# Kernel tuning notes

Hardware: AMD Instinct MI355X
Metric: run time of the kernel (lower is better)

The kernel has to match this reference:

```python
import jax, jax.numpy as jnp
import numpy as np

N = 50000      # nodes
E = 1000000    # edges (avg degree 20)
IN, H, OUT = 3, 128, 3


def setup_inputs() -> dict:
    key = jax.random.key(0)
    ks = jax.random.split(key, 12)
    pos = jax.random.normal(ks[0], (N, IN), dtype=jnp.float32)
    edge_index = jax.random.randint(ks[1], (2, E), 0, N, dtype=jnp.int64)
    dims = [(IN, H), (H, H), (H, H), (H, H), (H, OUT)]
    inp = {"pos": pos, "edge_index": edge_index}
    for i, (di, do) in enumerate(dims):
        inp[f"W{i}"] = jax.random.normal(ks[2 + 2 * i], (di, do), dtype=jnp.float32) / np.sqrt(di).astype(np.float32)
        inp[f"b{i}"] = jnp.zeros((do,), dtype=jnp.float32)
    return inp


def _gcn_conv(x, W, b, src, dst, norm):
    # PyG GCNConv: linear transform first, then normalized scatter-add, then bias
    h = x @ W                                  # [N, do]
    msg = h[src] * norm[:, None]               # gather + edge-normalize  [E+N, do]
    out = jax.ops.segment_sum(msg, dst, num_segments=N)  # scatter-add to targets
    return out + b


def reference(pos, edge_index, W0, b0, W1, b1, W2, b2, W3, b3, W4, b4):
    src, dst = edge_index[0], edge_index[1]
    loop = jnp.arange(N, dtype=src.dtype)
    src = jnp.concatenate([src, loop])         # add self-loops
    dst = jnp.concatenate([dst, loop])
    # symmetric normalization: deg computed on target nodes incl. self-loops
    deg = jax.ops.segment_sum(jnp.ones_like(src, dtype=pos.dtype), dst, num_segments=N)
    dis = jnp.where(deg > 0, jax.lax.rsqrt(jnp.maximum(deg, 1e-12)), 0.0)
    norm = dis[src] * dis[dst]                 # [E+N]

    Ws = [W0, W1, W2, W3, W4]
    bs = [b0, b1, b2, b3, b4]
    x = pos
    for i in range(4):                         # all but last layer: conv + SiLU
        x = jax.nn.silu(_gcn_conv(x, Ws[i], bs[i], src, dst, norm))
    return _gcn_conv(x, Ws[4], bs[4], src, dst, norm)
```

## Files before the change

### kernel.cpp

```cpp
#include <hip/hip_runtime.h>
#include <cstdint>
#include <cstddef>


#define NB_SPLIT 256
#define BUCKET_SHIFT 7

static __device__ __forceinline__ float silu_f(float x) {
  return x / (1.0f + __expf(-x));
}

__global__ __launch_bounds__(256) void k_prep(
    const int* __restrict__ e32, int* __restrict__ epack, int* __restrict__ cnt2,
    int E, int nbucket, int chunk) {
  __shared__ int hist[512];
  __shared__ int nz;
  const int w = blockIdx.x, t = threadIdx.x;
  for (int b = t; b < nbucket; b += 256) hist[b] = 0;
  if (t == 0) nz = 0;
  __syncthreads();
  if (e32[t * 2 + 1] != 0) nz = 1;
  __syncthreads();
  const int f = nz ? 0 : 1;
  const int i0 = w * chunk;
  const int i1 = min(E, i0 + chunk);
  for (int i = i0 + t; i < i1; i += 256) {
    int s, d;
    if (f) { s = e32[2 * i]; d = e32[2 * E + 2 * i]; }
    else   { s = e32[i];     d = e32[E + i]; }
    epack[i] = s | (d << 16);
    atomicAdd(&hist[d >> BUCKET_SHIFT], 1);
  }
  __syncthreads();
  for (int b = t; b < nbucket; b += 256) cnt2[b * NB_SPLIT + w] = hist[b];
}

__global__ void k_scan1(const int* __restrict__ cnt, int* __restrict__ outp,
                        int* __restrict__ bsum, int n) {
  __shared__ int wsum[4];
  const int t = threadIdx.x;
  const int base = blockIdx.x * 1024 + t * 4;
  int v0 = 0, v1 = 0, v2 = 0, v3 = 0;
  if (base + 0 < n) v0 = cnt[base + 0];
  if (base + 1 < n) v1 = cnt[base + 1];
  if (base + 2 < n) v2 = cnt[base + 2];
  if (base + 3 < n) v3 = cnt[base + 3];
  const int s = v0 + v1 + v2 + v3;
  int sc = s;
  const int lane = t & 63;
  #pragma unroll
  for (int o = 1; o < 64; o <<= 1) {
    int u = __shfl_up(sc, o);
    if (lane >= o) sc += u;
  }
  const int wid = t >> 6;
  if (lane == 63) wsum[wid] = sc;
  __syncthreads();
  int wbase = 0;
  for (int w = 0; w < wid; ++w) wbase += wsum[w];
  const int ex = wbase + sc - s;
  if (base + 0 < n) outp[base + 0] = ex;
  if (base + 1 < n) outp[base + 1] = ex + v0;
  if (base + 2 < n) outp[base + 2] = ex + v0 + v1;
  if (base + 3 < n) outp[base + 3] = ex + v0 + v1 + v2;
  if (t == 0) bsum[blockIdx.x] = wsum[0] + wsum[1] + wsum[2] + wsum[3];
}

__global__ __launch_bounds__(512) void k_sscan(
    int* __restrict__ arr, int n, int* __restrict__ tot0, int* __restrict__ tot1) {
  __shared__ int wsum[8];
  const int t = threadIdx.x;
  int v = (t < n) ? arr[t] : 0;
  int sc = v;
  const int lane = t & 63;
  #pragma unroll
  for (int o = 1; o < 64; o <<= 1) {
    int u = __shfl_up(sc, o);
    if (lane >= o) sc += u;
  }
  if (lane == 63) wsum[t >> 6] = sc;
  __syncthreads();
  int wb = 0;
  const int wid = t >> 6;
  for (int w = 0; w < wid; ++w) wb += wsum[w];
  const int ex = wb + sc - v;
  if (t < n) arr[t] = ex;
  if (t == n - 1) {
    int total = ex + v;
    if (tot0) *tot0 = total;
    if (tot1) *tot1 = total;
  }
}

__global__ void k_scanadd(int* __restrict__ arr, const int* __restrict__ bsum, int n) {
  int i = blockIdx.x * blockDim.x + threadIdx.x;
  if (i < n) arr[i] += bsum[i >> 10];
}

__global__ __launch_bounds__(256) void k_split(
    const int* __restrict__ epack, const int* __restrict__ off2,
    int* __restrict__ tmp, int E, int nbucket, int chunk) {
  __shared__ int cur[512];
  const int w = blockIdx.x, t = threadIdx.x;
  for (int b = t; b < nbucket; b += 256) cur[b] = off2[b * NB_SPLIT + w];
  __syncthreads();
  const int i0 = w * chunk;
  const int i1 = min(E, i0 + chunk);
  for (int i = i0 + t; i < i1; i += 256) {
    int p = epack[i];
    int b = (int)(((unsigned)p) >> (16 + BUCKET_SHIFT));
    int pos = atomicAdd(&cur[b], 1);
    tmp[pos] = p;
  }
}

__global__ __launch_bounds__(256) void k_csrA(
    const int* __restrict__ tmp, const int* __restrict__ off2,
    int* __restrict__ cnt_g, int* __restrict__ bpad, int E, int nbucket) {
  __shared__ int lcnt[128];
  __shared__ int tot;
  const int b = blockIdx.x, t = threadIdx.x;
  if (t < 128) lcnt[t] = 0;
  if (t == 0) tot = 0;
  __syncthreads();
  const int s0 = off2[b * NB_SPLIT];
  const int s1 = (b + 1 < nbucket) ? off2[(b + 1) * NB_SPLIT] : E;
  for (int i = s0 + t; i < s1; i += 256) {
    atomicAdd(&lcnt[((unsigned)tmp[i] >> 16) & 127u], 1);
  }
  __syncthreads();
  if (t < 128) {
    int v = lcnt[t];
    cnt_g[b * 128 + t] = v;
    atomicAdd(&tot, (v + 3) & ~3);
  }
  __syncthreads();
  if (t == 0) bpad[b] = tot;
}

__global__ __launch_bounds__(256) void k_csrB(
    const int* __restrict__ tmp, const int* __restrict__ off2,
    const int* __restrict__ cnt_g, const int* __restrict__ bpad,
    int* __restrict__ rowp, float* __restrict__ dis,
    unsigned short* __restrict__ col, int E, int nbucket, int N) {
  __shared__ int lcur[128];
  __shared__ int wtot;
  const int b = blockIdx.x, t = threadIdx.x;
  const int nb0 = b << BUCKET_SHIFT;
  const int nn = min(1 << BUCKET_SHIFT, N - nb0);
  int v = 0, pv = 0, sc = 0;
  if (t < 128) {
    v = cnt_g[b * 128 + t];
    pv = (v + 3) & ~3;
    sc = pv;
    #pragma unroll
    for (int o = 1; o < 64; o <<= 1) {
      int u = __shfl_up(sc, o);
      if ((t & 63) >= o) sc += u;
    }
    if (t == 63) wtot = sc;
  }
  __syncthreads();
  if (t < 128) {
    int ex = bpad[b] + ((t >= 64) ? wtot : 0) + sc - pv;
    lcur[t] = ex;
    if (t < nn) {
      rowp[nb0 + t] = ex;
      dis[nb0 + t] = rsqrtf((float)(v + 1));
      for (int p = ex + v; p < ex + pv; ++p) col[p] = (unsigned short)N;
    }
  }
  __syncthreads();
  const int s0 = off2[b * NB_SPLIT];
  const int s1 = (b + 1 < nbucket) ? off2[(b + 1) * NB_SPLIT] : E;
  for (int i = s0 + t; i < s1; i += 256) {
    unsigned p = (unsigned)tmp[i];
    int j = (int)((p >> 16) & ((1u << BUCKET_SHIFT) - 1));
    int pos = atomicAdd(&lcur[j], 1);
    col[pos] = (unsigned short)(p & 0xffffu);
  }
}

__global__ void k_zfill(float* __restrict__ bufA, float* __restrict__ bufB,
                        int N, int slStride) {
  const int t = threadIdx.x;
  const int bi = t >> 7, si = (t >> 4) & 7, ci = t & 15;
  float* bp = bi ? bufB : bufA;
  bp[(size_t)si * slStride + (size_t)N * 16 + ci] = 0.f;
}

template <int PRESCALE>
__global__ void k_agg3(const float* __restrict__ in3, float* __restrict__ out3,
                       const int* __restrict__ rowp,
                       const unsigned short* __restrict__ col,
                       const float* __restrict__ dis, const float* __restrict__ bias,
                       int n) {
  int i = blockIdx.x * blockDim.x + threadIdx.x;
  if (i >= n) return;
  const float di = dis[i];
  float a0, a1, a2;
  if (PRESCALE) {
    a0 = in3[i * 3 + 0] * di; a1 = in3[i * 3 + 1] * di; a2 = in3[i * 3 + 2] * di;
  } else {
    a0 = in3[i * 3 + 0]; a1 = in3[i * 3 + 1]; a2 = in3[i * 3 + 2];
  }
  const int e0 = rowp[i], e1 = rowp[i + 1];
  for (int e = e0; e < e1; ++e) {
    int s = col[e];
    if (s >= n) continue;
    if (PRESCALE) {
      float ds_ = dis[s];
      a0 += in3[s * 3 + 0] * ds_;
      a1 += in3[s * 3 + 1] * ds_;
      a2 += in3[s * 3 + 2] * ds_;
    } else {
      a0 += in3[s * 3 + 0];
      a1 += in3[s * 3 + 1];
      a2 += in3[s * 3 + 2];
    }
  }
  a0 *= di; a1 *= di; a2 *= di;
  if (!PRESCALE && bias) { a0 += bias[0]; a1 += bias[1]; a2 += bias[2]; }
  out3[i * 3 + 0] = a0;
  out3[i * 3 + 1] = a1;
  out3[i * 3 + 2] = a2;
}

__global__ void k_mm0(const float* __restrict__ y3, const float* __restrict__ W0,
                      const float* __restrict__ b0, const float* __restrict__ dis,
                      float* __restrict__ out, int n, int slStride) {
  int gid = blockIdx.x * blockDim.x + threadIdx.x;
  int node = gid >> 5;
  int c = (gid & 31) << 2;
  if (node >= n) return;
  float v0 = y3[node * 3 + 0], v1 = y3[node * 3 + 1], v2 = y3[node * 3 + 2];
  float4 a  = *reinterpret_cast<const float4*>(b0 + c);
  float4 w0 = *reinterpret_cast<const float4*>(W0 + 0 * 128 + c);
  float4 w1 = *reinterpret_cast<const float4*>(W0 + 1 * 128 + c);
  float4 w2 = *reinterpret_cast<const float4*>(W0 + 2 * 128 + c);
  a.x += v0 * w0.x + v1 * w1.x + v2 * w2.x;
  a.y += v0 * w0.y + v1 * w1.y + v2 * w2.y;
  a.z += v0 * w0.z + v1 * w1.z + v2 * w2.z;
  a.w += v0 * w0.w + v1 * w1.w + v2 * w2.w;
  const float d = dis[node];
  a.x = silu_f(a.x) * d; a.y = silu_f(a.y) * d;
  a.z = silu_f(a.z) * d; a.w = silu_f(a.w) * d;
  *reinterpret_cast<float4*>(out + (size_t)(c >> 4) * slStride +
                             (size_t)node * 16 + (c & 15)) = a;
}

__global__ __launch_bounds__(256) void k_agg_slice(
    const float* __restrict__ xs, float* __restrict__ y,
    const int* __restrict__ rowp, const unsigned short* __restrict__ col,
    const float* __restrict__ dis, int n, int slStride) {
  const int s = blockIdx.x & 7;
  const int nb = blockIdx.x >> 3;
  const int t = threadIdx.x;
  const int lane = t & 63;
  const int nsub = lane >> 3;
  const int ch = (lane >> 2) & 1;
  const int c4 = (lane & 3) << 2;
  const int node = nb * 32 + (t >> 6) * 8 + nsub;
  const bool valid = node < n;
  int e0 = 0, e1 = 0;
  if (valid) { e0 = rowp[node]; e1 = rowp[node + 1]; }
  const int P = e1 - e0;
  const int h = ((P >> 1) + 3) & ~3;
  const int eb = e0 + (ch ? h : 0);
  const int ee = ch ? e1 : (e0 + h);
  const float* __restrict__ xb = xs + (size_t)s * slStride + c4;

  float4 a0 = make_float4(0.f, 0.f, 0.f, 0.f);
  float4 a1 = make_float4(0.f, 0.f, 0.f, 0.f);
  float4 a2 = make_float4(0.f, 0.f, 0.f, 0.f);
  float4 a3 = make_float4(0.f, 0.f, 0.f, 0.f);
  for (int e = eb; e < ee; e += 4) {
    ushort4 idx = *reinterpret_cast<const ushort4*>(col + e);
    float4 v0 = *reinterpret_cast<const float4*>(xb + (size_t)idx.x * 16);
    float4 v1 = *reinterpret_cast<const float4*>(xb + (size_t)idx.y * 16);
    float4 v2 = *reinterpret_cast<const float4*>(xb + (size_t)idx.z * 16);
    float4 v3 = *reinterpret_cast<const float4*>(xb + (size_t)idx.w * 16);
    a0.x += v0.x; a0.y += v0.y; a0.z += v0.z; a0.w += v0.w;
    a1.x += v1.x; a1.y += v1.y; a1.z += v1.z; a1.w += v1.w;
    a2.x += v2.x; a2.y += v2.y; a2.z += v2.z; a2.w += v2.w;
    a3.x += v3.x; a3.y += v3.y; a3.z += v3.z; a3.w += v3.w;
  }
  a0.x += a1.x + a2.x + a3.x;
  a0.y += a1.y + a2.y + a3.y;
  a0.z += a1.z + a2.z + a3.z;
  a0.w += a1.w + a2.w + a3.w;
  a0.x += __shfl_xor(a0.x, 4);
  a0.y += __shfl_xor(a0.y, 4);
  a0.z += __shfl_xor(a0.z, 4);
  a0.w += __shfl_xor(a0.w, 4);
  if (valid && ch == 0) {
    float4 self = *reinterpret_cast<const float4*>(xb + (size_t)node * 16);
    const float d = dis[node];
    float4 r;
    r.x = (a0.x + self.x) * d;
    r.y = (a0.y + self.y) * d;
    r.z = (a0.z + self.z) * d;
    r.w = (a0.w + self.w) * d;
    *reinterpret_cast<float4*>(y + (size_t)s * slStride + (size_t)node * 16 + c4) = r;
  }
}

template <int PROJ>
__global__ __launch_bounds__(512, 4) void k_mm_w(
    const float* __restrict__ x, const float* __restrict__ W,
    const float* __restrict__ bias, const float* __restrict__ dis,
    float* __restrict__ out, const float* __restrict__ W4, int n, int slStride) {
  __shared__ float ws[128][128];
  const int t = threadIdx.x;
  #pragma unroll
  for (int it = 0; it < 8; ++it) {
    int i = t + it * 512;
    int k = i >> 5, b = i & 31;
    int slot = (b >> 1) | ((b & 1) << 4);
    *reinterpret_cast<float4*>(&ws[k][slot << 2]) =
        *reinterpret_cast<const float4*>(W + (size_t)i * 4);
  }
  __syncthreads();

  const int tc = t & 15;
  const int tr = (t >> 4) << 2;
  const int row0 = blockIdx.x * 128;

  int rb[4];
  #pragma unroll
  for (int r = 0; r < 4; ++r) {
    rb[r] = min(row0 + tr + r, n - 1) * 16;
  }

  float4 accA[4], accB[4];
  #pragma unroll
  for (int r = 0; r < 4; ++r) {
    accA[r] = make_float4(0.f, 0.f, 0.f, 0.f);
    accB[r] = make_float4(0.f, 0.f, 0.f, 0.f);
  }

  #pragma unroll 1
  for (int kk = 0; kk < 128; kk += 4) {
    const float* __restrict__ xk = x + (size_t)(kk >> 4) * slStride + (kk & 15);
    float4 xr[4];
    #pragma unroll
    for (int r = 0; r < 4; ++r) {
      xr[r] = *reinterpret_cast<const float4*>(xk + rb[r]);
    }
    #pragma unroll
    for (int j = 0; j < 4; ++j) {
      float4 wA = *reinterpret_cast<const float4*>(&ws[kk + j][tc << 2]);
      float4 wB = *reinterpret_cast<const float4*>(&ws[kk + j][64 + (tc << 2)]);
      #pragma unroll
      for (int r = 0; r < 4; ++r) {
        float xv = (j == 0) ? xr[r].x : (j == 1) ? xr[r].y : (j == 2) ? xr[r].z : xr[r].w;
        accA[r].x += xv * wA.x; accA[r].y += xv * wA.y;
        accA[r].z += xv * wA.z; accA[r].w += xv * wA.w;
        accB[r].x += xv * wB.x; accB[r].y += xv * wB.y;
        accB[r].z += xv * wB.z; accB[r].w += xv * wB.w;
      }
    }
  }

  float4 bbA = *reinterpret_cast<const float4*>(bias + tc * 8);
  float4 bbB = *reinterpret_cast<const float4*>(bias + tc * 8 + 4);
  if (PROJ) {
    float w4r[8][3];
    #pragma unroll
    for (int c = 0; c < 8; ++c) {
      w4r[c][0] = W4[(tc * 8 + c) * 3 + 0];
      w4r[c][1] = W4[(tc * 8 + c) * 3 + 1];
      w4r[c][2] = W4[(tc * 8 + c) * 3 + 2];
    }
    #pragma unroll
    for (int r = 0; r < 4; ++r) {
      int row = row0 + tr + r;
      float d = (row < n) ? dis[row] : 0.0f;
      float4 a = accA[r], b4 = accB[r];
      a.x = silu_f(a.x + bbA.x) * d;  a.y = silu_f(a.y + bbA.y) * d;
      a.z = silu_f(a.z + bbA.z) * d;  a.w = silu_f(a.w + bbA.w) * d;
      b4.x = silu_f(b4.x + bbB.x) * d; b4.y = silu_f(b4.y + bbB.y) * d;
      b4.z = silu_f(b4.z + bbB.z) * d; b4.w = silu_f(b4.w + bbB.w) * d;
      float p0 = a.x * w4r[0][0] + a.y * w4r[1][0] + a.z * w4r[2][0] + a.w * w4r[3][0]
               + b4.x * w4r[4][0] + b4.y * w4r[5][0] + b4.z * w4r[6][0] + b4.w * w4r[7][0];
      float p1 = a.x * w4r[0][1] + a.y * w4r[1][1] + a.z * w4r[2][1] + a.w * w4r[3][1]
               + b4.x * w4r[4][1] + b4.y * w4r[5][1] + b4.z * w4r[6][1] + b4.w * w4r[7][1];
      float p2 = a.x * w4r[0][2] + a.y * w4r[1][2] + a.z * w4r[2][2] + a.w * w4r[3][2]
               + b4.x * w4r[4][2] + b4.y * w4r[5][2] + b4.z * w4r[6][2] + b4.w * w4r[7][2];
      #pragma unroll
      for (int m = 8; m >= 1; m >>= 1) {
        p0 += __shfl_xor(p0, m);
        p1 += __shfl_xor(p1, m);
        p2 += __shfl_xor(p2, m);
      }
      if ((t & 15) == 0 && row < n) {
        out[row * 3 + 0] = p0;
        out[row * 3 + 1] = p1;
        out[row * 3 + 2] = p2;
      }
    }
  } else {
    #pragma unroll
    for (int r = 0; r < 4; ++r) {
      int row = row0 + tr + r;
      if (row < n) {
        float d = dis[row];
        float4 a = accA[r], b4 = accB[r];
        a.x = silu_f(a.x + bbA.x) * d;  a.y = silu_f(a.y + bbA.y) * d;
        a.z = silu_f(a.z + bbA.z) * d;  a.w = silu_f(a.w + bbA.w) * d;
        b4.x = silu_f(b4.x + bbB.x) * d; b4.y = silu_f(b4.y + bbB.y) * d;
        b4.z = silu_f(b4.z + bbB.z) * d; b4.w = silu_f(b4.w + bbB.w) * d;
        float* dst = out + (size_t)(tc >> 1) * slStride +
                     (size_t)row * 16 + ((tc & 1) << 3);
        *reinterpret_cast<float4*>(dst) = a;
        *reinterpret_cast<float4*>(dst + 4) = b4;
      }
    }
  }
}

extern "C" void kernel_launch(void* const* d_in, const int* in_sizes, int n_in,
                              void* d_out, int out_size, void* d_ws, size_t ws_size,
                              hipStream_t stream) {
  const float* pos = (const float*)d_in[0];
  const int* e32 = (const int*)d_in[1];
  const float* W[5] = {(const float*)d_in[2], (const float*)d_in[4], (const float*)d_in[6],
                       (const float*)d_in[8], (const float*)d_in[10]};
  const float* B[5] = {(const float*)d_in[3], (const float*)d_in[5], (const float*)d_in[7],
                       (const float*)d_in[9], (const float*)d_in[11]};
  float* out = (float*)d_out;

  const int N = in_sizes[0] / 3;
  const int E = in_sizes[1] / 2;
  const int NBUCKET = (N + (1 << BUCKET_SHIFT) - 1) >> BUCKET_SHIFT;
  const int M = NBUCKET * NB_SPLIT;
  const int chunk = (E + NB_SPLIT - 1) / NB_SPLIT;
  const int slStride = (N + 1) * 16;

  char* base = (char*)d_ws;
  size_t off = 0;
  auto alloc = [&](size_t bytes) -> void* {
    void* p = base + off;
    off += (bytes + 255) & ~(size_t)255;
    return p;
  };
  float* dis   = (float*)alloc((size_t)N * 4);
  int* rowp    = (int*)alloc((size_t)(N + 1) * 4);
  int* bsum2   = (int*)alloc(128 * 4);
  int* cnt_g   = (int*)alloc((size_t)NBUCKET * 128 * 4);
  int* bpad    = (int*)alloc((size_t)(NBUCKET + 1) * 4);
  int* cnt2    = (int*)alloc((size_t)M * 4);
  int* off2    = (int*)alloc((size_t)M * 4);
  unsigned short* col = (unsigned short*)alloc(((size_t)E + 4 * N) * 2);
  float* y3    = (float*)alloc((size_t)N * 3 * 4);
  float* bufA  = (float*)alloc((size_t)(N + 1) * 128 * 4);
  float* bufB  = (float*)alloc((size_t)(N + 1) * 128 * 4);
  int* epack = (int*)bufA;
  int* tmp   = (int*)bufB;

  const int nblk2 = (M + 1023) / 1024;

  k_prep<<<NB_SPLIT, 256, 0, stream>>>(e32, epack, cnt2, E, NBUCKET, chunk);
  k_scan1<<<nblk2, 256, 0, stream>>>(cnt2, off2, bsum2, M);
  k_sscan<<<1, 512, 0, stream>>>(bsum2, nblk2, nullptr, nullptr);
  k_scanadd<<<(M + 255) / 256, 256, 0, stream>>>(off2, bsum2, M);
  k_split<<<NB_SPLIT, 256, 0, stream>>>(epack, off2, tmp, E, NBUCKET, chunk);
  k_csrA<<<NBUCKET, 256, 0, stream>>>(tmp, off2, cnt_g, bpad, E, NBUCKET);
  k_sscan<<<1, 512, 0, stream>>>(bpad, NBUCKET, bpad + NBUCKET, rowp + N);
  k_csrB<<<NBUCKET, 256, 0, stream>>>(tmp, off2, cnt_g, bpad, rowp, dis, col, E, NBUCKET, N);
  k_zfill<<<1, 256, 0, stream>>>(bufA, bufB, N, slStride);

  k_agg3<1><<<(N + 255) / 256, 256, 0, stream>>>(pos, y3, rowp, col, dis, nullptr, N);
  k_mm0<<<(N * 32 + 255) / 256, 256, 0, stream>>>(y3, W[0], B[0], dis, bufA, N, slStride);

  const int agg_grid = ((N + 31) / 32) * 8;
  const int mm_grid = (N + 127) / 128;
  for (int l = 1; l <= 2; ++l) {
    k_agg_slice<<<agg_grid, 256, 0, stream>>>(bufA, bufB, rowp, col, dis, N, slStride);
    k_mm_w<0><<<mm_grid, 512, 0, stream>>>(bufB, W[l], B[l], dis, bufA, nullptr, N, slStride);
  }

  k_agg_slice<<<agg_grid, 256, 0, stream>>>(bufA, bufB, rowp, col, dis, N, slStride);
  k_mm_w<1><<<mm_grid, 512, 0, stream>>>(bufB, W[3], B[3], dis, y3, W[4], N, slStride);

  k_agg3<0><<<(N + 255) / 256, 256, 0, stream>>>(y3, out, rowp, col, dis, B[4], N);

  (void)n_in; (void)out_size; (void)ws_size;
}
```

Measured before the change: 320.5 us.

## Simplify CSR build with global bucket atomics and fewer kernel launches

Replaces the per-block bucket count matrix and its three-kernel multi-level scan with global atomic bucket totals, a single small scan, and per-block atomic reservation of bucket ranges inside the split kernel. It merges the two CSR kernels into one by padding each bucket with fixed slack so bucket column offsets no longer need a second scan. It also folds the zero-fill kernel into the first aggregation kernel. The aim is to cut launch count and the scan traffic in the graph preprocessing. In exchange, the split kernel reads the edges twice, and the order of edges within a bucket now depends on atomic timing.

```diff
diff --git a/kernel.cpp b/kernel.cpp
--- a/kernel.cpp
+++ b/kernel.cpp
@@ -5,13 +5,14 @@
 
 #define NB_SPLIT 256
 #define BUCKET_SHIFT 7
+#define BSLACK 512
 
 static __device__ __forceinline__ float silu_f(float x) {
   return x / (1.0f + __expf(-x));
 }
 
 __global__ __launch_bounds__(256) void k_prep(
-    const int* __restrict__ e32, int* __restrict__ epack, int* __restrict__ cnt2,
+    const int* __restrict__ e32, int* __restrict__ epack, int* __restrict__ bT,
     int E, int nbucket, int chunk) {
   __shared__ int hist[512];
   __shared__ int nz;
@@ -32,42 +33,14 @@
     atomicAdd(&hist[d >> BUCKET_SHIFT], 1);
   }
   __syncthreads();
-  for (int b = t; b < nbucket; b += 256) cnt2[b * NB_SPLIT + w] = hist[b];
-}
-
-__global__ void k_scan1(const int* __restrict__ cnt, int* __restrict__ outp,
-                        int* __restrict__ bsum, int n) {
-  __shared__ int wsum[4];
-  const int t = threadIdx.x;
-  const int base = blockIdx.x * 1024 + t * 4;
-  int v0 = 0, v1 = 0, v2 = 0, v3 = 0;
-  if (base + 0 < n) v0 = cnt[base + 0];
-  if (base + 1 < n) v1 = cnt[base + 1];
-  if (base + 2 < n) v2 = cnt[base + 2];
-  if (base + 3 < n) v3 = cnt[base + 3];
-  const int s = v0 + v1 + v2 + v3;
-  int sc = s;
-  const int lane = t & 63;
-  #pragma unroll
-  for (int o = 1; o < 64; o <<= 1) {
-    int u = __shfl_up(sc, o);
-    if (lane >= o) sc += u;
-  }
-  const int wid = t >> 6;
-  if (lane == 63) wsum[wid] = sc;
-  __syncthreads();
-  int wbase = 0;
-  for (int w = 0; w < wid; ++w) wbase += wsum[w];
-  const int ex = wbase + sc - s;
-  if (base + 0 < n) outp[base + 0] = ex;
-  if (base + 1 < n) outp[base + 1] = ex + v0;
-  if (base + 2 < n) outp[base + 2] = ex + v0 + v1;
-  if (base + 3 < n) outp[base + 3] = ex + v0 + v1 + v2;
-  if (t == 0) bsum[blockIdx.x] = wsum[0] + wsum[1] + wsum[2] + wsum[3];
-}
-
-__global__ __launch_bounds__(512) void k_sscan(
-    int* __restrict__ arr, int n, int* __restrict__ tot0, int* __restrict__ tot1) {
+  for (int b = t; b < nbucket; b += 256) {
+    int h = hist[b];
+    if (h) atomicAdd(&bT[b], h);
+  }
+}
+
+__global__ __launch_bounds__(512) void k_sscan2(
+    int* __restrict__ arr, int* __restrict__ cpy, int n) {
   __shared__ int wsum[8];
   const int t = threadIdx.x;
   int v = (t < n) ? arr[t] : 0;
@@ -84,28 +57,29 @@
   const int wid = t >> 6;
   for (int w = 0; w < wid; ++w) wb += wsum[w];
   const int ex = wb + sc - v;
-  if (t < n) arr[t] = ex;
-  if (t == n - 1) {
-    int total = ex + v;
-    if (tot0) *tot0 = total;
-    if (tot1) *tot1 = total;
-  }
-}
-
-__global__ void k_scanadd(int* __restrict__ arr, const int* __restrict__ bsum, int n) {
-  int i = blockIdx.x * blockDim.x + threadIdx.x;
-  if (i < n) arr[i] += bsum[i >> 10];
+  if (t < n) { arr[t] = ex; cpy[t] = ex; }
+  if (t == n - 1) arr[n] = ex + v;
 }
 
 __global__ __launch_bounds__(256) void k_split(
-    const int* __restrict__ epack, const int* __restrict__ off2,
+    const int* __restrict__ epack, int* __restrict__ gcur,
     int* __restrict__ tmp, int E, int nbucket, int chunk) {
   __shared__ int cur[512];
   const int w = blockIdx.x, t = threadIdx.x;
-  for (int b = t; b < nbucket; b += 256) cur[b] = off2[b * NB_SPLIT + w];
+  for (int b = t; b < nbucket; b += 256) cur[b] = 0;
   __syncthreads();
   const int i0 = w * chunk;
   const int i1 = min(E, i0 + chunk);
+  for (int i = i0 + t; i < i1; i += 256) {
+    int b = (int)(((unsigned)epack[i]) >> (16 + BUCKET_SHIFT));
+    atomicAdd(&cur[b], 1);
+  }
+  __syncthreads();
+  for (int b = t; b < nbucket; b += 256) {
+    int h = cur[b];
+    cur[b] = h ? atomicAdd(&gcur[b], h) : 0;
+  }
+  __syncthreads();
   for (int i = i0 + t; i < i1; i += 256) {
     int p = epack[i];
     int b = (int)(((unsigned)p) >> (16 + BUCKET_SHIFT));
@@ -114,43 +88,28 @@
   }
 }
 
-__global__ __launch_bounds__(256) void k_csrA(
-    const int* __restrict__ tmp, const int* __restrict__ off2,
-    int* __restrict__ cnt_g, int* __restrict__ bpad, int E, int nbucket) {
+__global__ __launch_bounds__(256) void k_csr(
+    const int* __restrict__ tmp, const int* __restrict__ bbase,
+    int* __restrict__ rowp, float* __restrict__ dis,
+    unsigned short* __restrict__ col, int nbucket, int N) {
   __shared__ int lcnt[128];
-  __shared__ int tot;
-  const int b = blockIdx.x, t = threadIdx.x;
-  if (t < 128) lcnt[t] = 0;
-  if (t == 0) tot = 0;
-  __syncthreads();
-  const int s0 = off2[b * NB_SPLIT];
-  const int s1 = (b + 1 < nbucket) ? off2[(b + 1) * NB_SPLIT] : E;
-  for (int i = s0 + t; i < s1; i += 256) {
-    atomicAdd(&lcnt[((unsigned)tmp[i] >> 16) & 127u], 1);
-  }
-  __syncthreads();
-  if (t < 128) {
-    int v = lcnt[t];
-    cnt_g[b * 128 + t] = v;
-    atomicAdd(&tot, (v + 3) & ~3);
-  }
-  __syncthreads();
-  if (t == 0) bpad[b] = tot;
-}
-
-__global__ __launch_bounds__(256) void k_csrB(
-    const int* __restrict__ tmp, const int* __restrict__ off2,
-    const int* __restrict__ cnt_g, const int* __restrict__ bpad,
-    int* __restrict__ rowp, float* __restrict__ dis,
-    unsigned short* __restrict__ col, int E, int nbucket, int N) {
   __shared__ int lcur[128];
   __shared__ int wtot;
+  __shared__ int ptot;
   const int b = blockIdx.x, t = threadIdx.x;
   const int nb0 = b << BUCKET_SHIFT;
   const int nn = min(1 << BUCKET_SHIFT, N - nb0);
+  if (t < 128) lcnt[t] = 0;
+  __syncthreads();
+  const int s0 = bbase[b], s1 = bbase[b + 1];
+  for (int i = s0 + t; i < s1; i += 256) {
+    atomicAdd(&lcnt[((unsigned)tmp[i] >> 16) & 127u], 1);
+  }
+  __syncthreads();
+  const int cbase = ((s0 + 3) & ~3) + b * BSLACK;
   int v = 0, pv = 0, sc = 0;
   if (t < 128) {
-    v = cnt_g[b * 128 + t];
+    v = lcnt[t];
     pv = (v + 3) & ~3;
     sc = pv;
     #pragma unroll
@@ -162,17 +121,20 @@
   }
   __syncthreads();
   if (t < 128) {
-    int ex = bpad[b] + ((t >= 64) ? wtot : 0) + sc - pv;
+    int ex = cbase + ((t >= 64) ? wtot : 0) + sc - pv;
     lcur[t] = ex;
     if (t < nn) {
       rowp[nb0 + t] = ex;
       dis[nb0 + t] = rsqrtf((float)(v + 1));
       for (int p = ex + v; p < ex + pv; ++p) col[p] = (unsigned short)N;
     }
-  }
-  __syncthreads();
-  const int s0 = off2[b * NB_SPLIT];
-  const int s1 = (b + 1 < nbucket) ? off2[(b + 1) * NB_SPLIT] : E;
+    if (t == 127) ptot = ex + pv;
+  }
+  __syncthreads();
+  const int nxt = (b + 1 < nbucket)
+      ? (((bbase[b + 1] + 3) & ~3) + (b + 1) * BSLACK) : ptot;
+  if (b == nbucket - 1 && t == 0) rowp[N] = ptot;
+  for (int p = ptot + t; p < nxt; p += 256) col[p] = (unsigned short)N;
   for (int i = s0 + t; i < s1; i += 256) {
     unsigned p = (unsigned)tmp[i];
     int j = (int)((p >> 16) & ((1u << BUCKET_SHIFT) - 1));
@@ -181,20 +143,19 @@
   }
 }
 
-__global__ void k_zfill(float* __restrict__ bufA, float* __restrict__ bufB,
-                        int N, int slStride) {
-  const int t = threadIdx.x;
-  const int bi = t >> 7, si = (t >> 4) & 7, ci = t & 15;
-  float* bp = bi ? bufB : bufA;
-  bp[(size_t)si * slStride + (size_t)N * 16 + ci] = 0.f;
-}
-
 template <int PRESCALE>
 __global__ void k_agg3(const float* __restrict__ in3, float* __restrict__ out3,
                        const int* __restrict__ rowp,
                        const unsigned short* __restrict__ col,
                        const float* __restrict__ dis, const float* __restrict__ bias,
-                       int n) {
+                       float* __restrict__ zA, float* __restrict__ zB,
+                       int slStride, int n) {
+  if (PRESCALE && blockIdx.x == 0) {
+    const int t = threadIdx.x;
+    const int bi = t >> 7, si = (t >> 4) & 7, ci = t & 15;
+    float* bp = bi ? zB : zA;
+    bp[(size_t)si * slStride + (size_t)n * 16 + ci] = 0.f;
+  }
   int i = blockIdx.x * blockDim.x + threadIdx.x;
   if (i >= n) return;
   const float di = dis[i];
@@ -433,7 +394,6 @@
   const int N = in_sizes[0] / 3;
   const int E = in_sizes[1] / 2;
   const int NBUCKET = (N + (1 << BUCKET_SHIFT) - 1) >> BUCKET_SHIFT;
-  const int M = NBUCKET * NB_SPLIT;
   const int chunk = (E + NB_SPLIT - 1) / NB_SPLIT;
   const int slStride = (N + 1) * 16;
 
@@ -446,31 +406,24 @@
   };
   float* dis   = (float*)alloc((size_t)N * 4);
   int* rowp    = (int*)alloc((size_t)(N + 1) * 4);
-  int* bsum2   = (int*)alloc(128 * 4);
-  int* cnt_g   = (int*)alloc((size_t)NBUCKET * 128 * 4);
-  int* bpad    = (int*)alloc((size_t)(NBUCKET + 1) * 4);
-  int* cnt2    = (int*)alloc((size_t)M * 4);
-  int* off2    = (int*)alloc((size_t)M * 4);
-  unsigned short* col = (unsigned short*)alloc(((size_t)E + 4 * N) * 2);
+  int* bT      = (int*)alloc((size_t)(NBUCKET + 1) * 4);
+  int* gcur    = (int*)alloc((size_t)NBUCKET * 4);
+  unsigned short* col =
+      (unsigned short*)alloc(((size_t)E + (size_t)NBUCKET * BSLACK + 16) * 2);
   float* y3    = (float*)alloc((size_t)N * 3 * 4);
   float* bufA  = (float*)alloc((size_t)(N + 1) * 128 * 4);
   float* bufB  = (float*)alloc((size_t)(N + 1) * 128 * 4);
   int* epack = (int*)bufA;
   int* tmp   = (int*)bufB;
 
-  const int nblk2 = (M + 1023) / 1024;
-
-  k_prep<<<NB_SPLIT, 256, 0, stream>>>(e32, epack, cnt2, E, NBUCKET, chunk);
-  k_scan1<<<nblk2, 256, 0, stream>>>(cnt2, off2, bsum2, M);
-  k_sscan<<<1, 512, 0, stream>>>(bsum2, nblk2, nullptr, nullptr);
-  k_scanadd<<<(M + 255) / 256, 256, 0, stream>>>(off2, bsum2, M);
-  k_split<<<NB_SPLIT, 256, 0, stream>>>(epack, off2, tmp, E, NBUCKET, chunk);
-  k_csrA<<<NBUCKET, 256, 0, stream>>>(tmp, off2, cnt_g, bpad, E, NBUCKET);
-  k_sscan<<<1, 512, 0, stream>>>(bpad, NBUCKET, bpad + NBUCKET, rowp + N);
-  k_csrB<<<NBUCKET, 256, 0, stream>>>(tmp, off2, cnt_g, bpad, rowp, dis, col, E, NBUCKET, N);
-  k_zfill<<<1, 256, 0, stream>>>(bufA, bufB, N, slStride);
-
-  k_agg3<1><<<(N + 255) / 256, 256, 0, stream>>>(pos, y3, rowp, col, dis, nullptr, N);
+  hipMemsetAsync(bT, 0, (size_t)(NBUCKET + 1) * 4, stream);
+  k_prep<<<NB_SPLIT, 256, 0, stream>>>(e32, epack, bT, E, NBUCKET, chunk);
+  k_sscan2<<<1, 512, 0, stream>>>(bT, gcur, NBUCKET);
+  k_split<<<NB_SPLIT, 256, 0, stream>>>(epack, gcur, tmp, E, NBUCKET, chunk);
+  k_csr<<<NBUCKET, 256, 0, stream>>>(tmp, bT, rowp, dis, col, NBUCKET, N);
+
+  k_agg3<1><<<(N + 255) / 256, 256, 0, stream>>>(
+      pos, y3, rowp, col, dis, nullptr, bufA, bufB, slStride, N);
   k_mm0<<<(N * 32 + 255) / 256, 256, 0, stream>>>(y3, W[0], B[0], dis, bufA, N, slStride);
 
   const int agg_grid = ((N + 31) / 32) * 8;
@@ -483,7 +436,8 @@
   k_agg_slice<<<agg_grid, 256, 0, stream>>>(bufA, bufB, rowp, col, dis, N, slStride);
   k_mm_w<1><<<mm_grid, 512, 0, stream>>>(bufB, W[3], B[3], dis, y3, W[4], N, slStride);
 
-  k_agg3<0><<<(N + 255) / 256, 256, 0, stream>>>(y3, out, rowp, col, dis, B[4], N);
+  k_agg3<0><<<(N + 255) / 256, 256, 0, stream>>>(
+      y3, out, rowp, col, dis, B[4], nullptr, nullptr, slStride, N);
 
   (void)n_in; (void)out_size; (void)ws_size;
 }
```

Measured after the change: 590.8 us. 84.3% more time.
